# Kernel tuning notes

Measured on AMD Instinct MI355X. Metric: run time of the kernel, lower is better.

Reference implementation:

```python
import jax, jax.numpy as jnp
import numpy as np

T, N, C, D, S = 512, 32, 1296, 512, 30
NORM_SCALE = 32.0
NEGINF = -1e9


def setup_inputs() -> dict:
    key = jax.random.key(0)
    k1, k2, k3, k4, k5 = jax.random.split(key, 5)
    feats = jax.random.normal(k1, (T * N, D), dtype=jnp.float32)
    classifier_weight = jax.random.normal(k2, (D, C), dtype=jnp.float32)
    labeling = jax.random.randint(k3, (N, S), 1, C)  # targets cannot be blank(0)
    logit_lgts = (T - jax.random.randint(k4, (N,), 0, 32)).astype(jnp.int32)
    labeling_lgts = (S - jax.random.randint(k5, (N,), 0, 5)).astype(jnp.int32)
    return dict(feats=feats, classifier_weight=classifier_weight,
                labeling=labeling, logit_lgts=logit_lgts, labeling_lgts=labeling_lgts)


def _ctc_loss(log_probs, labels, in_lens, lab_lens):
    # log_probs: (T, N, C); labels: (N, S); blank = 0; reduction = 'sum'
    Tt, Nn, Cc = log_probs.shape
    Ss = labels.shape[1]
    L = 2 * Ss + 1
    # extended labeling: blank, l1, blank, l2, ..., blank  -> (N, L)
    ext = jnp.zeros((Nn, L), dtype=labels.dtype).at[:, 1::2].set(labels)
    # gather per-state log-probs: (T, N, L)
    lp_ext = jnp.take_along_axis(log_probs, jnp.broadcast_to(ext[None], (Tt, Nn, L)), axis=2)
    # skip transition s-2 -> s allowed iff s > 1 and ext[s] != ext[s-2]
    skip_ok = jnp.concatenate(
        [jnp.zeros((Nn, 2), dtype=bool), ext[:, 2:] != ext[:, :-2]], axis=1)
    alpha0 = (jnp.full((Nn, L), NEGINF, dtype=log_probs.dtype)
              .at[:, 0].set(lp_ext[0, :, 0])
              .at[:, 1].set(lp_ext[0, :, 1]))

    def step(alpha, inp):
        lp_t, t = inp  # lp_t: (N, L)
        a1 = alpha
        a2 = jnp.pad(alpha[:, :-1], ((0, 0), (1, 0)), constant_values=NEGINF)
        a3 = jnp.where(skip_ok,
                       jnp.pad(alpha[:, :-2], ((0, 0), (2, 0)), constant_values=NEGINF),
                       NEGINF)
        new = jax.nn.logsumexp(jnp.stack([a1, a2, a3], axis=0), axis=0) + lp_t
        # freeze alpha once t reaches a sample's input length
        alpha = jnp.where((t < in_lens)[:, None], new, alpha)
        return alpha, None

    alpha, _ = jax.lax.scan(step, alpha0, (lp_ext[1:], jnp.arange(1, Tt)))
    Ln = 2 * lab_lens + 1  # (N,)
    last = jnp.take_along_axis(alpha, (Ln - 1)[:, None], axis=1)[:, 0]
    last2 = jnp.take_along_axis(alpha, (Ln - 2)[:, None], axis=1)[:, 0]
    nll = -jnp.logaddexp(last, last2)
    return jnp.sum(nll)


def reference(feats, classifier_weight, labeling, logit_lgts, labeling_lgts):
    # RadialCTC: cosine logits with norm_scale, then CTC on log-softmax.
    w_n = classifier_weight / jnp.linalg.norm(classifier_weight, axis=0, keepdims=True)  # (D, C)
    f_n = feats / jnp.linalg.norm(feats, axis=1, keepdims=True)  # (T*N, D)
    logits = NORM_SCALE * (f_n @ w_n)  # (T*N, C)
    log_probs = jax.nn.log_softmax(logits.reshape(T, N, C), axis=-1)
    return _ctc_loss(log_probs, labeling, logit_lgts, labeling_lgts)
```

## Files before the change

### kernel.cpp

```cpp
#include <hip/hip_runtime.h>
#include <stdint.h>
#include <stddef.h>


typedef _Float16 f16;
typedef _Float16 f16x8 __attribute__((ext_vector_type(8)));
typedef float f32x4 __attribute__((ext_vector_type(4)));
typedef __attribute__((address_space(1))) void* as1_void_ptr;
typedef __attribute__((address_space(3))) void* as3_void_ptr;

#define TT 512
#define NN 32
#define CC 1296
#define DD 512
#define SS 30
#define CP 1408
#define LL 61
#define NEGINF (-1e9f)
#define NORM_SCALE 32.0f
#define LOG2E 1.4426950408889634f
#define LN2   0.6931471805599453f

__device__ __forceinline__ float fexp2(float x) { return __builtin_amdgcn_exp2f(x); }
__device__ __forceinline__ float flog2(float x) { return __builtin_amdgcn_logf(x); }

__device__ __forceinline__ double dpp_sr1_zero64(double x) {
    long long b = __double_as_longlong(x);
    int lo = (int)(b & 0xFFFFFFFFLL);
    int hi = (int)(b >> 32);
    int lo2 = __builtin_amdgcn_update_dpp(0, lo, 0x138, 0xF, 0xF, false);
    int hi2 = __builtin_amdgcn_update_dpp(0, hi, 0x138, 0xF, 0xF, false);
    return __longlong_as_double(((long long)hi2 << 32) |
                                (unsigned long long)(unsigned int)lo2);
}
template <int CTRL>
__device__ __forceinline__ int dpp_imax_level(int m) {
    int t = __builtin_amdgcn_update_dpp(0, m, CTRL, 0xF, 0xF, false);
    return m > t ? m : t;
}

__global__ void colnorm_kernel(const float* __restrict__ W, float* __restrict__ ssq) {
    int c = blockIdx.x * 64 + threadIdx.x;
    if (c >= CC) return;
    int d0 = blockIdx.y * 64;
    float ss = 0.f;
    #pragma unroll 8
    for (int d = d0; d < d0 + 64; ++d) {
        float v = W[(size_t)d * CC + c];
        ss += v * v;
    }
    atomicAdd(&ssq[c], ss);
}

__global__ void wt_kernel(const float* __restrict__ W, const float* __restrict__ ssq,
                          f16* __restrict__ wt) {
    int idx = blockIdx.x * 256 + threadIdx.x;
    int c = idx >> 9, d = idx & 511;
    float v = 0.f;
    if (c < CC) v = W[(size_t)d * CC + c] * rsqrtf(ssq[c]);
    wt[idx] = (f16)v;
}

__global__ __launch_bounds__(256) void fnorm_kernel(const float* __restrict__ feats,
                                                    f16* __restrict__ fn) {
    int wv = (blockIdx.x * 256 + threadIdx.x) >> 6;
    int lane = threadIdx.x & 63;
    const float4* src = (const float4*)(feats + (size_t)wv * DD) + lane * 2;
    float4 a = src[0], b = src[1];
    float ss = a.x*a.x + a.y*a.y + a.z*a.z + a.w*a.w
             + b.x*b.x + b.y*b.y + b.z*b.z + b.w*b.w;
    #pragma unroll
    for (int off = 32; off; off >>= 1) ss += __shfl_xor(ss, off);
    float r = rsqrtf(ss);
    f16x8 o;
    o[0]=(f16)(a.x*r); o[1]=(f16)(a.y*r); o[2]=(f16)(a.z*r); o[3]=(f16)(a.w*r);
    o[4]=(f16)(b.x*r); o[5]=(f16)(b.y*r); o[6]=(f16)(b.z*r); o[7]=(f16)(b.w*r);
    *(f16x8*)(fn + (size_t)wv * DD + lane * 8) = o;
}

__global__ __launch_bounds__(256) void gemm_sumexp_kernel(const f16* __restrict__ A,
                                                          const f16* __restrict__ B,
                                                          float* __restrict__ sumexp) {
    __shared__ __align__(16) f16 As[128 * 32];
    __shared__ __align__(16) f16 Bs[128 * 32];
    int bm = blockIdx.x, bn = blockIdx.y;
    int tid = threadIdx.x;
    int w = tid >> 6, lane = tid & 63;
    int wm = w >> 1, wn = w & 1;
    int lm = lane & 15, hi = lane >> 4;
    int sw = (lm >> 1) & 3;
    f32x4 acc[4][4];
    f32x4 zero = {0.f, 0.f, 0.f, 0.f};
    #pragma unroll
    for (int i = 0; i < 4; ++i)
        #pragma unroll
        for (int j = 0; j < 4; ++j) acc[i][j] = zero;

    for (int kb = 0; kb < 16; ++kb) {
        #pragma unroll
        for (int p = 0; p < 2; ++p) {
            int s = p * 256 + tid;
            int row = s >> 2;
            int ch = (s & 3) ^ ((row >> 1) & 3);
            const f16* ga = A + (size_t)(bm * 128 + row) * DD + kb * 32 + ch * 8;
            const f16* gb = B + (size_t)(bn * 128 + row) * DD + kb * 32 + ch * 8;
            __builtin_amdgcn_global_load_lds((as1_void_ptr)ga,
                (as3_void_ptr)&As[(p * 256 + w * 64) * 8], 16, 0, 0);
            __builtin_amdgcn_global_load_lds((as1_void_ptr)gb,
                (as3_void_ptr)&Bs[(p * 256 + w * 64) * 8], 16, 0, 0);
        }
        __syncthreads();
        f16x8 af[4], bf[4];
        #pragma unroll
        for (int i = 0; i < 4; ++i)
            af[i] = *(const f16x8*)&As[(wm * 64 + i * 16 + lm) * 32 + (hi ^ sw) * 8];
        #pragma unroll
        for (int j = 0; j < 4; ++j)
            bf[j] = *(const f16x8*)&Bs[(wn * 64 + j * 16 + lm) * 32 + (hi ^ sw) * 8];
        #pragma unroll
        for (int i = 0; i < 4; ++i)
            #pragma unroll
            for (int j = 0; j < 4; ++j)
                acc[i][j] = __builtin_amdgcn_mfma_f32_16x16x32_f16(af[i], bf[j], acc[i][j], 0, 0, 0);
        __syncthreads();
    }
    #pragma unroll
    for (int i = 0; i < 4; ++i) {
        float rs[4] = {0.f, 0.f, 0.f, 0.f};
        #pragma unroll
        for (int j = 0; j < 4; ++j) {
            int c = bn * 128 + wn * 64 + j * 16 + lm;
            bool ok = (c < CC);
            #pragma unroll
            for (int r = 0; r < 4; ++r)
                rs[r] += ok ? fexp2(acc[i][j][r] * (NORM_SCALE * LOG2E)) : 0.f;
        }
        #pragma unroll
        for (int off = 1; off < 16; off <<= 1) {
            #pragma unroll
            for (int r = 0; r < 4; ++r) rs[r] += __shfl_xor(rs[r], off);
        }
        if (lm == 0) {
            int rowb = bm * 128 + wm * 64 + i * 16 + hi * 4;
            #pragma unroll
            for (int r = 0; r < 4; ++r) atomicAdd(&sumexp[rowb + r], rs[r]);
        }
    }
}

__global__ __launch_bounds__(256) void gather_kernel(const f16* __restrict__ fn,
                                                     const f16* __restrict__ wt,
                                                     const float* __restrict__ sumexp,
                                                     const int* __restrict__ labels,
                                                     float* __restrict__ lp_lab) {
    __shared__ __align__(16) f16 Bs[16 * 32 * 32];
    __shared__ __align__(16) f16 As[16 * 64 * 32];
    __shared__ float ls2[64];
    int n = blockIdx.x, t0 = blockIdx.y * 64;
    int tid = threadIdx.x;
    int w = tid >> 6, lane = tid & 63;
    int lm = lane & 15, hi = lane >> 4;
    int sw = (lm >> 1) & 3;

    #pragma unroll
    for (int it = 0; it < 8; ++it) {
        int s = it * 256 + tid;
        int row = (s >> 2) & 31;
        int ch = (s & 3) ^ ((row >> 1) & 3);
        int cls = (row == 0 || row > SS) ? 0 : labels[n * SS + row - 1];
        const f16* gb = wt + (size_t)cls * DD + (s >> 7) * 32 + ch * 8;
        __builtin_amdgcn_global_load_lds((as1_void_ptr)gb,
            (as3_void_ptr)&Bs[(it * 256 + w * 64) * 8], 16, 0, 0);
    }
    #pragma unroll
    for (int it = 0; it < 16; ++it) {
        int s = it * 256 + tid;
        int kb = s >> 8, row = (s >> 2) & 63;
        int ch = (s & 3) ^ ((row >> 1) & 3);
        const f16* ga = fn + (size_t)((t0 + row) * NN + n) * DD + kb * 32 + ch * 8;
        __builtin_amdgcn_global_load_lds((as1_void_ptr)ga,
            (as3_void_ptr)&As[(it * 256 + w * 64) * 8], 16, 0, 0);
    }
    if (tid < 64) ls2[tid] = flog2(sumexp[(size_t)(t0 + tid) * NN + n]);
    __syncthreads();

    f32x4 acc[2];
    acc[0] = (f32x4){0.f, 0.f, 0.f, 0.f};
    acc[1] = (f32x4){0.f, 0.f, 0.f, 0.f};
    #pragma unroll
    for (int kb = 0; kb < 16; ++kb) {
        f16x8 af  = *(const f16x8*)&As[kb * 2048 + (w * 16 + lm) * 32 + (hi ^ sw) * 8];
        f16x8 bf0 = *(const f16x8*)&Bs[kb * 1024 + lm * 32 + (hi ^ sw) * 8];
        f16x8 bf1 = *(const f16x8*)&Bs[kb * 1024 + (16 + lm) * 32 + (hi ^ sw) * 8];
        acc[0] = __builtin_amdgcn_mfma_f32_16x16x32_f16(af, bf0, acc[0], 0, 0, 0);
        acc[1] = __builtin_amdgcn_mfma_f32_16x16x32_f16(af, bf1, acc[1], 0, 0, 0);
    }
    #pragma unroll
    for (int jn = 0; jn < 2; ++jn) {
        int j = jn * 16 + lm;
        if (j >= 31) continue;
        float* dst = lp_lab + ((size_t)n * 31 + j) * TT + t0;
        #pragma unroll
        for (int r = 0; r < 4; ++r) {
            int tl = w * 16 + hi * 4 + r;
            dst[tl] = acc[jn][r] * (NORM_SCALE * LOG2E) - ls2[tl];
        }
    }
}

__global__ void ctc_kernel(const float* __restrict__ lp_lab, const int* __restrict__ labels,
                           const int* __restrict__ in_lens, const int* __restrict__ lab_lens,
                           float* __restrict__ nll) {
    int n = blockIdx.x;
    int s = threadIdx.x;
    bool valid = s < LL;
    int ext = (valid && (s & 1)) ? labels[n * SS + (s >> 1)] : 0;
    int jmap = (valid && (s & 1)) ? ((s >> 1) + 1) : 0;
    int ext2 = __shfl_up(ext, 2);
    double skipd = ((s >= 2) && valid && (ext != ext2)) ? 1.0 : 0.0;
    int Tin = in_lens[n];
    const float4* g0 = (const float4*)(lp_lab + ((size_t)n * 31 + jmap) * TT);

    float4 cur = g0[0];
    float4 nxt = g0[1];
    float4 nx2 = g0[2];
    double beta = (s <= 1) ? (double)fexp2(cur.x) : 0.0;
    int Mi = 0;

    auto stepL = [&](float lp) {
        double P = (double)fexp2(lp);
        double b1 = dpp_sr1_zero64(beta);
        double b2 = dpp_sr1_zero64(b1);
        beta = (beta + b1 + b2 * skipd) * P;
    };
    auto renorm = [&]() {
        int h = (int)(__double_as_longlong(beta) >> 32);
        h = dpp_imax_level<0x111>(h);
        h = dpp_imax_level<0x112>(h);
        h = dpp_imax_level<0x114>(h);
        h = dpp_imax_level<0x118>(h);
        int r0 = __builtin_amdgcn_readlane(h, 15);
        int r1 = __builtin_amdgcn_readlane(h, 31);
        int r2 = __builtin_amdgcn_readlane(h, 47);
        int r3 = __builtin_amdgcn_readlane(h, 63);
        int mx = max(max(r0, r1), max(r2, r3));
        int e11 = mx >> 20;
        double scale = __longlong_as_double((long long)(2046 - e11) << 52);
        beta *= scale;
        Mi += e11 - 1023;
    };

    stepL(cur.y); stepL(cur.z); stepL(cur.w);
    renorm();
    int remaining = Tin - 4;
    int g = 1;
    while (remaining >= 4) {
        cur = nxt; nxt = nx2;
        int gi = g + 2; if (gi > 127) gi = 127;
        nx2 = g0[gi];
        stepL(cur.x); stepL(cur.y); stepL(cur.z); stepL(cur.w);
        renorm();
        remaining -= 4; ++g;
    }
    cur = nxt;
    if (remaining > 0) stepL(cur.x);
    if (remaining > 1) stepL(cur.y);
    if (remaining > 2) stepL(cur.z);

    int Ln = 2 * lab_lens[n] + 1;
    double last  = __shfl(beta, Ln - 1);
    double last2 = __shfl(beta, Ln - 2);
    double sm = last + last2;
    long long bb = __double_as_longlong(sm);
    int e = (int)(bb >> 52) - 1023;
    double mant = __longlong_as_double((bb & 0xFFFFFFFFFFFFFLL) | (1023LL << 52));
    float v = -(flog2((float)mant) + (float)(e + Mi)) * LN2;
    if (s == 0) nll[n] = v;
}

__global__ void reduce_kernel(const float* __restrict__ nll, float* __restrict__ out) {
    int s = threadIdx.x;
    float v = (s < NN) ? nll[s] : 0.f;
    #pragma unroll
    for (int off = 32; off; off >>= 1) v += __shfl_xor(v, off);
    if (s == 0) out[0] = v;
}

extern "C" void kernel_launch(void* const* d_in, const int* in_sizes, int n_in,
                              void* d_out, int out_size, void* d_ws, size_t ws_size,
                              hipStream_t stream) {
    const float* feats        = (const float*)d_in[0];
    const float* W            = (const float*)d_in[1];
    const int*   labeling     = (const int*)d_in[2];
    const int*   logit_lgts   = (const int*)d_in[3];
    const int*   labeling_lgts= (const int*)d_in[4];
    float* out = (float*)d_out;
    char* ws = (char*)d_ws;

    size_t off = 0;
    f16*   wt     = (f16*)(ws + off);   off += (size_t)CP * DD * 2;
    f16*   fn     = (f16*)(ws + off);   off += (size_t)TT * NN * DD * 2;
    float* ssq    = (float*)(ws + off); off += 1312 * 4;
    float* sumexp = (float*)(ws + off); off += (size_t)TT * NN * 4;
    float* lp_lab = (float*)(ws + off); off += (size_t)NN * 31 * TT * 4;
    float* nllb   = (float*)(ws + off); off += 64 * 4;

    hipMemsetAsync(ssq, 0, 1312 * 4, stream);
    hipMemsetAsync(sumexp, 0, (size_t)TT * NN * 4, stream);

    colnorm_kernel<<<dim3((CC + 63) / 64, 8), 64, 0, stream>>>(W, ssq);
    wt_kernel<<<(CP * DD) / 256, 256, 0, stream>>>(W, ssq, wt);
    fnorm_kernel<<<(TT * NN) / 4, 256, 0, stream>>>(feats, fn);
    gemm_sumexp_kernel<<<dim3(TT * NN / 128, CP / 128), 256, 0, stream>>>(fn, wt, sumexp);
    gather_kernel<<<dim3(NN, TT / 64), 256, 0, stream>>>(fn, wt, sumexp, labeling, lp_lab);
    ctc_kernel<<<NN, 64, 0, stream>>>(lp_lab, labeling, logit_lgts, labeling_lgts, nllb);
    reduce_kernel<<<1, 64, 0, stream>>>(nllb, out);

    (void)in_sizes; (void)n_in; (void)out_size; (void)ws_size;
}
```

Measured before the change: 164.3 us.

## Fuse GEMM-sumexp and label gather into one launch, defer log-normalizer to CTC

The log-softmax normalizer is separated from per-step emission scores. Because every CTC path consumes exactly one emission per valid time step, the sum of log2(sumexp) over t < Tin can be subtracted once at the end of the CTC kernel. That removes the gather kernel's dependency on the finished sumexp, so the GEMM and gather blocks now run as one merged launch, saving a kernel boundary and letting the two phases overlap. The gather path now streams A per k-block instead of preloading it, and the row-sum shuffles are replaced with DPP adds. Risk: the DPP row_shr reduction pattern must still leave the correct total in lane lm==0, and the CTC kernel gets a small serial tail.

After: 167.4 us. No clear change (+1.9%).

```diff
diff --git a/kernel.cpp b/kernel.cpp
--- a/kernel.cpp
+++ b/kernel.cpp
@@ -20,6 +20,8 @@
 #define NORM_SCALE 32.0f
 #define LOG2E 1.4426950408889634f
 #define LN2   0.6931471805599453f
+#define GEMM_BLOCKS (11 * 128)
+#define GATH_BLOCKS (NN * (TT / 64))
 
 __device__ __forceinline__ float fexp2(float x) { return __builtin_amdgcn_exp2f(x); }
 __device__ __forceinline__ float flog2(float x) { return __builtin_amdgcn_logf(x); }
@@ -37,6 +39,12 @@
 __device__ __forceinline__ int dpp_imax_level(int m) {
     int t = __builtin_amdgcn_update_dpp(0, m, CTRL, 0xF, 0xF, false);
     return m > t ? m : t;
+}
+template <int CTRL>
+__device__ __forceinline__ float dpp_add_level(float m) {
+    float t = __int_as_float(__builtin_amdgcn_update_dpp(
+        0, __float_as_int(m), CTRL, 0xF, 0xF, false));
+    return m + t;
 }
 
 __global__ void colnorm_kernel(const float* __restrict__ W, float* __restrict__ ssq) {
@@ -78,137 +86,133 @@
     *(f16x8*)(fn + (size_t)wv * DD + lane * 8) = o;
 }
 
-__global__ __launch_bounds__(256) void gemm_sumexp_kernel(const f16* __restrict__ A,
-                                                          const f16* __restrict__ B,
-                                                          float* __restrict__ sumexp) {
-    __shared__ __align__(16) f16 As[128 * 32];
-    __shared__ __align__(16) f16 Bs[128 * 32];
-    int bm = blockIdx.x, bn = blockIdx.y;
-    int tid = threadIdx.x;
-    int w = tid >> 6, lane = tid & 63;
-    int wm = w >> 1, wn = w & 1;
-    int lm = lane & 15, hi = lane >> 4;
-    int sw = (lm >> 1) & 3;
-    f32x4 acc[4][4];
-    f32x4 zero = {0.f, 0.f, 0.f, 0.f};
-    #pragma unroll
-    for (int i = 0; i < 4; ++i)
-        #pragma unroll
-        for (int j = 0; j < 4; ++j) acc[i][j] = zero;
-
-    for (int kb = 0; kb < 16; ++kb) {
-        #pragma unroll
-        for (int p = 0; p < 2; ++p) {
-            int s = p * 256 + tid;
-            int row = s >> 2;
-            int ch = (s & 3) ^ ((row >> 1) & 3);
-            const f16* ga = A + (size_t)(bm * 128 + row) * DD + kb * 32 + ch * 8;
-            const f16* gb = B + (size_t)(bn * 128 + row) * DD + kb * 32 + ch * 8;
-            __builtin_amdgcn_global_load_lds((as1_void_ptr)ga,
-                (as3_void_ptr)&As[(p * 256 + w * 64) * 8], 16, 0, 0);
-            __builtin_amdgcn_global_load_lds((as1_void_ptr)gb,
-                (as3_void_ptr)&Bs[(p * 256 + w * 64) * 8], 16, 0, 0);
-        }
-        __syncthreads();
-        f16x8 af[4], bf[4];
-        #pragma unroll
-        for (int i = 0; i < 4; ++i)
-            af[i] = *(const f16x8*)&As[(wm * 64 + i * 16 + lm) * 32 + (hi ^ sw) * 8];
-        #pragma unroll
-        for (int j = 0; j < 4; ++j)
-            bf[j] = *(const f16x8*)&Bs[(wn * 64 + j * 16 + lm) * 32 + (hi ^ sw) * 8];
-        #pragma unroll
-        for (int i = 0; i < 4; ++i)
-            #pragma unroll
-            for (int j = 0; j < 4; ++j)
-                acc[i][j] = __builtin_amdgcn_mfma_f32_16x16x32_f16(af[i], bf[j], acc[i][j], 0, 0, 0);
-        __syncthreads();
-    }
-    #pragma unroll
-    for (int i = 0; i < 4; ++i) {
-        float rs[4] = {0.f, 0.f, 0.f, 0.f};
-        #pragma unroll
-        for (int j = 0; j < 4; ++j) {
-            int c = bn * 128 + wn * 64 + j * 16 + lm;
-            bool ok = (c < CC);
-            #pragma unroll
-            for (int r = 0; r < 4; ++r)
-                rs[r] += ok ? fexp2(acc[i][j][r] * (NORM_SCALE * LOG2E)) : 0.f;
-        }
-        #pragma unroll
-        for (int off = 1; off < 16; off <<= 1) {
-            #pragma unroll
-            for (int r = 0; r < 4; ++r) rs[r] += __shfl_xor(rs[r], off);
-        }
-        if (lm == 0) {
-            int rowb = bm * 128 + wm * 64 + i * 16 + hi * 4;
-            #pragma unroll
-            for (int r = 0; r < 4; ++r) atomicAdd(&sumexp[rowb + r], rs[r]);
-        }
-    }
-}
-
-__global__ __launch_bounds__(256) void gather_kernel(const f16* __restrict__ fn,
-                                                     const f16* __restrict__ wt,
-                                                     const float* __restrict__ sumexp,
-                                                     const int* __restrict__ labels,
-                                                     float* __restrict__ lp_lab) {
-    __shared__ __align__(16) f16 Bs[16 * 32 * 32];
-    __shared__ __align__(16) f16 As[16 * 64 * 32];
-    __shared__ float ls2[64];
-    int n = blockIdx.x, t0 = blockIdx.y * 64;
+__global__ __launch_bounds__(256) void gg_kernel(const f16* __restrict__ A,
+                                                 const f16* __restrict__ B,
+                                                 float* __restrict__ sumexp,
+                                                 const int* __restrict__ labels,
+                                                 float* __restrict__ lp_lab) {
+    __shared__ __align__(16) f16 smem[18432];
+    int blk = blockIdx.x;
     int tid = threadIdx.x;
     int w = tid >> 6, lane = tid & 63;
     int lm = lane & 15, hi = lane >> 4;
     int sw = (lm >> 1) & 3;
 
-    #pragma unroll
-    for (int it = 0; it < 8; ++it) {
-        int s = it * 256 + tid;
-        int row = (s >> 2) & 31;
-        int ch = (s & 3) ^ ((row >> 1) & 3);
-        int cls = (row == 0 || row > SS) ? 0 : labels[n * SS + row - 1];
-        const f16* gb = wt + (size_t)cls * DD + (s >> 7) * 32 + ch * 8;
-        __builtin_amdgcn_global_load_lds((as1_void_ptr)gb,
-            (as3_void_ptr)&Bs[(it * 256 + w * 64) * 8], 16, 0, 0);
+    if (blk < GEMM_BLOCKS) {
+        int bm = blk / 11, bn = blk % 11;
+        f16* As = smem;
+        f16* Bs = smem + 4096;
+        int wm = w >> 1, wn = w & 1;
+        f32x4 acc[4][4];
+        f32x4 zero = {0.f, 0.f, 0.f, 0.f};
+        #pragma unroll
+        for (int i = 0; i < 4; ++i)
+            #pragma unroll
+            for (int j = 0; j < 4; ++j) acc[i][j] = zero;
+
+        for (int kb = 0; kb < 16; ++kb) {
+            #pragma unroll
+            for (int p = 0; p < 2; ++p) {
+                int s = p * 256 + tid;
+                int row = s >> 2;
+                int ch = (s & 3) ^ ((row >> 1) & 3);
+                const f16* ga = A + (size_t)(bm * 128 + row) * DD + kb * 32 + ch * 8;
+                const f16* gb = B + (size_t)(bn * 128 + row) * DD + kb * 32 + ch * 8;
+                __builtin_amdgcn_global_load_lds((as1_void_ptr)ga,
+                    (as3_void_ptr)&As[(p * 256 + w * 64) * 8], 16, 0, 0);
+                __builtin_amdgcn_global_load_lds((as1_void_ptr)gb,
+                    (as3_void_ptr)&Bs[(p * 256 + w * 64) * 8], 16, 0, 0);
+            }
+            __syncthreads();
+            f16x8 af[4], bf[4];
+            #pragma unroll
+            for (int i = 0; i < 4; ++i)
+                af[i] = *(const f16x8*)&As[(wm * 64 + i * 16 + lm) * 32 + (hi ^ sw) * 8];
+            #pragma unroll
+            for (int j = 0; j < 4; ++j)
+                bf[j] = *(const f16x8*)&Bs[(wn * 64 + j * 16 + lm) * 32 + (hi ^ sw) * 8];
+            #pragma unroll
+            for (int i = 0; i < 4; ++i)
+                #pragma unroll
+                for (int j = 0; j < 4; ++j)
+                    acc[i][j] = __builtin_amdgcn_mfma_f32_16x16x32_f16(af[i], bf[j], acc[i][j], 0, 0, 0);
+            __syncthreads();
+        }
+        #pragma unroll
+        for (int i = 0; i < 4; ++i) {
+            float rs[4] = {0.f, 0.f, 0.f, 0.f};
+            #pragma unroll
+            for (int j = 0; j < 4; ++j) {
+                int c = bn * 128 + wn * 64 + j * 16 + lm;
+                bool ok = (c < CC);
+                #pragma unroll
+                for (int r = 0; r < 4; ++r)
+                    rs[r] += ok ? fexp2(acc[i][j][r] * (NORM_SCALE * LOG2E)) : 0.f;
+            }
+            #pragma unroll
+            for (int r = 0; r < 4; ++r) {
+                float m = rs[r];
+                m = dpp_add_level<0x128>(m);
+                m = dpp_add_level<0x124>(m);
+                m = dpp_add_level<0x122>(m);
+                m = dpp_add_level<0x121>(m);
+                rs[r] = m;
+            }
+            if (lm == 0) {
+                int rowb = bm * 128 + wm * 64 + i * 16 + hi * 4;
+                #pragma unroll
+                for (int r = 0; r < 4; ++r) atomicAdd(&sumexp[rowb + r], rs[r]);
+            }
+        }
+    } else {
+        int idx = blk - GEMM_BLOCKS;
+        int n = idx & 31, t0 = (idx >> 5) * 64;
+        f16* Bg = smem;
+        f16* Ag = smem + 16384;
+        #pragma unroll
+        for (int it = 0; it < 8; ++it) {
+            int s = it * 256 + tid;
+            int row = (s >> 2) & 31;
+            int ch = (s & 3) ^ ((row >> 1) & 3);
+            int cls = (row == 0 || row > SS) ? 0 : labels[n * SS + row - 1];
+            const f16* gb = B + (size_t)cls * DD + (s >> 7) * 32 + ch * 8;
+            __builtin_amdgcn_global_load_lds((as1_void_ptr)gb,
+                (as3_void_ptr)&Bg[(it * 256 + w * 64) * 8], 16, 0, 0);
+        }
+        f32x4 acc[2];
+        acc[0] = (f32x4){0.f, 0.f, 0.f, 0.f};
+        acc[1] = (f32x4){0.f, 0.f, 0.f, 0.f};
+        for (int kb = 0; kb < 16; ++kb) {
+            int row = tid >> 2;
+            int ch = (tid & 3) ^ ((row >> 1) & 3);
+            const f16* ga = A + (size_t)((t0 + row) * NN + n) * DD + kb * 32 + ch * 8;
+            __builtin_amdgcn_global_load_lds((as1_void_ptr)ga,
+                (as3_void_ptr)&Ag[(w * 64) * 8], 16, 0, 0);
+            __syncthreads();
+            f16x8 af  = *(const f16x8*)&Ag[(w * 16 + lm) * 32 + (hi ^ sw) * 8];
+            f16x8 bf0 = *(const f16x8*)&Bg[kb * 1024 + lm * 32 + (hi ^ sw) * 8];
+            f16x8 bf1 = *(const f16x8*)&Bg[kb * 1024 + (16 + lm) * 32 + (hi ^ sw) * 8];
+            acc[0] = __builtin_amdgcn_mfma_f32_16x16x32_f16(af, bf0, acc[0], 0, 0, 0);
+            acc[1] = __builtin_amdgcn_mfma_f32_16x16x32_f16(af, bf1, acc[1], 0, 0, 0);
+            __syncthreads();
+        }
+        #pragma unroll
+        for (int jn = 0; jn < 2; ++jn) {
+            int j = jn * 16 + lm;
+            if (j >= 31) continue;
+            float* dst = lp_lab + ((size_t)n * 31 + j) * TT + t0;
+            #pragma unroll
+            for (int r = 0; r < 4; ++r) {
+                int tl = w * 16 + hi * 4 + r;
+                dst[tl] = acc[jn][r] * (NORM_SCALE * LOG2E);
+            }
+        }
     }
-    #pragma unroll
-    for (int it = 0; it < 16; ++it) {
-        int s = it * 256 + tid;
-        int kb = s >> 8, row = (s >> 2) & 63;
-        int ch = (s & 3) ^ ((row >> 1) & 3);
-        const f16* ga = fn + (size_t)((t0 + row) * NN + n) * DD + kb * 32 + ch * 8;
-        __builtin_amdgcn_global_load_lds((as1_void_ptr)ga,
-            (as3_void_ptr)&As[(it * 256 + w * 64) * 8], 16, 0, 0);
-    }
-    if (tid < 64) ls2[tid] = flog2(sumexp[(size_t)(t0 + tid) * NN + n]);
-    __syncthreads();
-
-    f32x4 acc[2];
-    acc[0] = (f32x4){0.f, 0.f, 0.f, 0.f};
-    acc[1] = (f32x4){0.f, 0.f, 0.f, 0.f};
-    #pragma unroll
-    for (int kb = 0; kb < 16; ++kb) {
-        f16x8 af  = *(const f16x8*)&As[kb * 2048 + (w * 16 + lm) * 32 + (hi ^ sw) * 8];
-        f16x8 bf0 = *(const f16x8*)&Bs[kb * 1024 + lm * 32 + (hi ^ sw) * 8];
-        f16x8 bf1 = *(const f16x8*)&Bs[kb * 1024 + (16 + lm) * 32 + (hi ^ sw) * 8];
-        acc[0] = __builtin_amdgcn_mfma_f32_16x16x32_f16(af, bf0, acc[0], 0, 0, 0);
-        acc[1] = __builtin_amdgcn_mfma_f32_16x16x32_f16(af, bf1, acc[1], 0, 0, 0);
-    }
-    #pragma unroll
-    for (int jn = 0; jn < 2; ++jn) {
-        int j = jn * 16 + lm;
-        if (j >= 31) continue;
-        float* dst = lp_lab + ((size_t)n * 31 + j) * TT + t0;
-        #pragma unroll
-        for (int r = 0; r < 4; ++r) {
-            int tl = w * 16 + hi * 4 + r;
-            dst[tl] = acc[jn][r] * (NORM_SCALE * LOG2E) - ls2[tl];
-        }
-    }
-}
-
-__global__ void ctc_kernel(const float* __restrict__ lp_lab, const int* __restrict__ labels,
+}
+
+__global__ void ctc_kernel(const float* __restrict__ lp_lab,
+                           const float* __restrict__ sumexp,
+                           const int* __restrict__ labels,
                            const int* __restrict__ in_lens, const int* __restrict__ lab_lens,
                            float* __restrict__ nll) {
     int n = blockIdx.x;
@@ -267,6 +271,15 @@
     if (remaining > 1) stepL(cur.y);
     if (remaining > 2) stepL(cur.z);
 
+    float S = 0.f;
+    #pragma unroll
+    for (int k = 0; k < 8; ++k) {
+        int t = (k << 6) + s;
+        if (t < Tin) S += flog2(sumexp[t * NN + n]);
+    }
+    #pragma unroll
+    for (int off = 32; off; off >>= 1) S += __shfl_xor(S, off);
+
     int Ln = 2 * lab_lens[n] + 1;
     double last  = __shfl(beta, Ln - 1);
     double last2 = __shfl(beta, Ln - 2);
@@ -274,7 +287,7 @@
     long long bb = __double_as_longlong(sm);
     int e = (int)(bb >> 52) - 1023;
     double mant = __longlong_as_double((bb & 0xFFFFFFFFFFFFFLL) | (1023LL << 52));
-    float v = -(flog2((float)mant) + (float)(e + Mi)) * LN2;
+    float v = -(flog2((float)mant) + (float)(e + Mi) - S) * LN2;
     if (s == 0) nll[n] = v;
 }
 
@@ -311,9 +324,8 @@
     colnorm_kernel<<<dim3((CC + 63) / 64, 8), 64, 0, stream>>>(W, ssq);
     wt_kernel<<<(CP * DD) / 256, 256, 0, stream>>>(W, ssq, wt);
     fnorm_kernel<<<(TT * NN) / 4, 256, 0, stream>>>(feats, fn);
-    gemm_sumexp_kernel<<<dim3(TT * NN / 128, CP / 128), 256, 0, stream>>>(fn, wt, sumexp);
-    gather_kernel<<<dim3(NN, TT / 64), 256, 0, stream>>>(fn, wt, sumexp, labeling, lp_lab);
-    ctc_kernel<<<NN, 64, 0, stream>>>(lp_lab, labeling, logit_lgts, labeling_lgts, nllb);
+    gg_kernel<<<GEMM_BLOCKS + GATH_BLOCKS, 256, 0, stream>>>(fn, wt, sumexp, labeling, lp_lab);
+    ctc_kernel<<<NN, 64, 0, stream>>>(lp_lab, sumexp, labeling, logit_lgts, labeling_lgts, nllb);
     reduce_kernel<<<1, 64, 0, stream>>>(nllb, out);
 
     (void)in_sizes; (void)n_in; (void)out_size; (void)ws_size;
```
